# Performance work log

Measured on AMD Instinct MI355X. Metric: run time of the kernel, lower is better.

Reference implementation:

```python
import jax, jax.numpy as jnp
import numpy as np

N_SENT, B, S, D = 256, 512, 128, 1024
L, LATENT = 10331, 101  # int(sqrt(10331)) == 101


def setup_inputs() -> dict:
    key = jax.random.key(0)
    ks = jax.random.split(key, 16)
    inv = 1.0 / np.sqrt(D)
    return {
        'elmo_outputs': jax.random.normal(ks[0], (N_SENT, S, D), jnp.float32),
        'men_mask': jax.random.randint(ks[1], (B, S), 0, 2).astype(jnp.float32),
        'ctx_mask': jax.random.randint(ks[2], (B, S), 0, 2).astype(jnp.float32),
        'dist': jax.random.uniform(ks[3], (B, S), jnp.float32),
        'gathers': jax.random.randint(ks[4], (B,), 0, N_SENT),
        # nn.Linear weights, stored [out, in] as in torch
        'W_men_m': jax.random.normal(ks[5], (D, D), jnp.float32) * inv,
        'W_men_o': jax.random.normal(ks[6], (1, D), jnp.float32) * inv,
        'W_ctx_c': jax.random.normal(ks[7], (D, D), jnp.float32) * inv,
        'W_ctx_m': jax.random.normal(ks[8], (D, D), jnp.float32) * inv,
        'w_ctx_d': jax.random.normal(ks[9], (D,), jnp.float32),  # Linear(1, D) weight [D,1] squeezed
        'W_ctx_o': jax.random.normal(ks[10], (1, D), jnp.float32) * inv,
        'W_out': jax.random.normal(ks[11], (L, 2 * D), jnp.float32) * (1.0 / np.sqrt(2 * D)),
        'W_f2l': jax.random.normal(ks[12], (LATENT, 2 * D), jnp.float32) * (1.0 / np.sqrt(2 * D)),
        'W_l2l': jax.random.normal(ks[13], (L, LATENT), jnp.float32) * (1.0 / np.sqrt(LATENT)),
        'latent_scalar': jnp.array(0.1, jnp.float32),
    }


def reference(elmo_outputs, men_mask, ctx_mask, dist, gathers,
              W_men_m, W_men_o, W_ctx_c, W_ctx_m, w_ctx_d, W_ctx_o,
              W_out, W_f2l, W_l2l, latent_scalar):
    NEG = -10000.0
    # gather: sentence reps -> mention rows, [B, S, D]
    x = elmo_outputs[gathers]
    # mention additive attention
    men_h = jnp.tanh(jnp.einsum('bsd,ed->bse', x, W_men_m))
    men_score = jnp.einsum('bse,oe->bso', men_h, W_men_o)  # [B,S,1]
    men_score = men_score + (1.0 - men_mask[:, :, None]) * NEG
    men_attn = jax.nn.softmax(men_score, axis=1)
    men_repr = jnp.sum(x * men_attn, axis=1)  # [B, D]
    # context additive attention (dropout layers are identity in eval)
    ctx_h = jnp.tanh(
        jnp.einsum('bsd,ed->bse', x, W_ctx_c)
        + jnp.einsum('bd,ed->be', men_repr, W_ctx_m)[:, None, :]
        + dist[:, :, None] * w_ctx_d
    )
    ctx_score = jnp.einsum('bse,oe->bso', ctx_h, W_ctx_o)
    ctx_score = ctx_score + (1.0 - ctx_mask[:, :, None]) * NEG
    ctx_attn = jax.nn.softmax(ctx_score, axis=1)
    ctx_repr = jnp.sum(x * ctx_attn, axis=1)  # [B, D]
    final_repr = jnp.concatenate([men_repr, ctx_repr], axis=1)  # [B, 2D]
    outputs = final_repr @ W_out.T  # [B, L]
    latent_label = final_repr @ W_f2l.T  # [B, latent]
    outputs_latent = latent_label @ W_l2l.T  # [B, L]
    outputs = outputs + latent_scalar * outputs_latent
    return outputs, outputs_latent
```

## Files before the change

kernel.cpp:

```cpp
#include <hip/hip_runtime.h>
#include <hip/hip_bf16.h>

typedef __bf16 bf16x8 __attribute__((ext_vector_type(8)));
typedef float f32x4 __attribute__((ext_vector_type(4)));
typedef unsigned short u16x8 __attribute__((ext_vector_type(8)));

#define DEV __device__ __forceinline__

static constexpr int N_SENTC = 256, BB = 512, SS = 128, DD = 1024;
static constexpr int LL = 10331, LATENT = 101;
static constexpr int LPAD = 10368;
static constexpr int LATPAD = 128;

DEV float bf2f(unsigned short u) {
  unsigned v = (unsigned)u << 16;
  return __builtin_bit_cast(float, v);
}
DEV unsigned short f2bf(float f) {
  unsigned u = __builtin_bit_cast(unsigned, f);
  unsigned lsb = (u >> 16) & 1u;
  u += 0x7fffu + lsb;
  return (unsigned short)(u >> 16);
}

DEV void stage8(unsigned short* dst, const float* src) {
  float4 a = *(const float4*)src;
  float4 b = *(const float4*)(src + 4);
  unsigned short t[8];
  t[0] = f2bf(a.x); t[1] = f2bf(a.y); t[2] = f2bf(a.z); t[3] = f2bf(a.w);
  t[4] = f2bf(b.x); t[5] = f2bf(b.y); t[6] = f2bf(b.z); t[7] = f2bf(b.w);
  *(uint4*)dst = *(uint4*)t;
}

DEV void gl_lds16(const unsigned short* g, unsigned short* l) {
  __builtin_amdgcn_global_load_lds(
      (const __attribute__((address_space(1))) unsigned int*)g,
      (__attribute__((address_space(3))) unsigned int*)l, 16, 0, 0);
}

__global__ __launch_bounds__(256) void k_cvt(
    const float* __restrict__ src, unsigned short* __restrict__ dst, int n4) {
  for (int i = blockIdx.x * 256 + threadIdx.x; i < n4; i += gridDim.x * 256) {
    float4 v = ((const float4*)src)[i];
    unsigned short t[4] = {f2bf(v.x), f2bf(v.y), f2bf(v.z), f2bf(v.w)};
    ((uint2*)dst)[i] = *(const uint2*)t;
  }
}

__global__ __launch_bounds__(256) void k_cvt_pad(
    const float* __restrict__ src, unsigned short* __restrict__ dst,
    int srcR, int srcC, int dstC, int total) {
  for (int i = blockIdx.x * 256 + threadIdx.x; i < total; i += gridDim.x * 256) {
    int r = i / dstC, c = i - r * dstC;
    dst[i] = (r < srcR && c < srcC) ? f2bf(src[(size_t)r * srcC + c]) : (unsigned short)0;
  }
}

__global__ __launch_bounds__(512) void k_mc_gemm8(
    const unsigned short* __restrict__ Xb, const unsigned short* __restrict__ Wmb,
    const unsigned short* __restrict__ Wcb, const float* __restrict__ wo,
    float* __restrict__ score, unsigned short* __restrict__ Hc) {
  __shared__ __align__(16) unsigned short lds[2][2][2][8192];
  const int bid = blockIdx.x;
  const int lbid = (bid & 7) * 128 + (bid >> 3);
  const int colTile = lbid & 7, rowTile = lbid >> 3;
  const int rowBase = rowTile * 256;
  const bool isMen = colTile < 4;
  const unsigned short* __restrict__ Bsrc = isMen ? Wmb : Wcb;
  const int bcolBase = (colTile & 3) * 256;
  const int tid = threadIdx.x, w = tid >> 6, lane = tid & 63;
  const int lm = lane & 15, lq = lane >> 4;
  const int wr = w >> 2, wc = w & 3;
  const int stRow = w * 16 + (lane >> 2);
  const int stCol = ((lane & 3) * 8) ^ ((lane >> 5) << 4);
  const unsigned short* aSrc = Xb + (size_t)(rowBase + stRow) * 1024 + stCol;
  const unsigned short* bSrc = Bsrc + (size_t)(bcolBase + stRow) * 1024 + stCol;
  const int rdCol = (lq * 16) ^ ((lane & 8) ? 32 : 0);
  const int aoff = (wr * 16 + lm) * 64 + rdCol;
  const int boff = (wc * 16 + lm) * 64 + rdCol;
  f32x4 acc[8][4] = {};

  auto ST = [&](int op, int h, int kt, int buf) {
    const unsigned short* s = (op ? bSrc : aSrc) + (size_t)h * 131072 + kt * 64;
    unsigned short* d = &lds[buf][op][h][w * 512];
    gl_lds16(s, d);
    gl_lds16(s + 32, d + 4096);
  };

  ST(0, 0, 0, 0); ST(1, 0, 0, 0); ST(0, 1, 0, 0); ST(1, 1, 0, 0);
  ST(0, 0, 1, 1); ST(1, 0, 1, 1); ST(0, 1, 1, 1);
  asm volatile("s_waitcnt vmcnt(6)" ::: "memory");
  __builtin_amdgcn_s_barrier();

  bf16x8 af[4][2], bfr[4][2];
  for (int kt = 0; kt < 16; ++kt) {
    const int buf = kt & 1;
    const char* A0 = (const char*)&lds[buf][0][0][0];
    const char* A1 = (const char*)&lds[buf][0][1][0];
    const char* B0 = (const char*)&lds[buf][1][0][0];
    const char* B1 = (const char*)&lds[buf][1][1][0];
#pragma unroll
    for (int m = 0; m < 4; ++m)
#pragma unroll
      for (int ks = 0; ks < 2; ++ks)
        af[m][ks] = *(const bf16x8*)(A0 + aoff + m * 2048 + ks * 8192);
#pragma unroll
    for (int n = 0; n < 2; ++n)
#pragma unroll
      for (int ks = 0; ks < 2; ++ks)
        bfr[n][ks] = *(const bf16x8*)(B0 + boff + n * 4096 + ks * 8192);
    if (kt + 1 < 16) ST(1, 1, kt + 1, buf ^ 1);
    __builtin_amdgcn_s_barrier();
    __builtin_amdgcn_s_setprio(1);
#pragma unroll
    for (int m = 0; m < 4; ++m)
#pragma unroll
      for (int n = 0; n < 2; ++n)
#pragma unroll
        for (int ks = 0; ks < 2; ++ks)
          acc[m][n] = __builtin_amdgcn_mfma_f32_16x16x32_bf16(af[m][ks], bfr[n][ks], acc[m][n], 0, 0, 0);
    __builtin_amdgcn_s_setprio(0);
    __builtin_amdgcn_s_barrier();
#pragma unroll
    for (int n = 0; n < 2; ++n)
#pragma unroll
      for (int ks = 0; ks < 2; ++ks)
        bfr[2 + n][ks] = *(const bf16x8*)(B1 + boff + n * 4096 + ks * 8192);
    if (kt + 2 < 16) ST(0, 0, kt + 2, buf);
    __builtin_amdgcn_s_barrier();
    __builtin_amdgcn_s_setprio(1);
#pragma unroll
    for (int m = 0; m < 4; ++m)
#pragma unroll
      for (int n = 0; n < 2; ++n)
#pragma unroll
        for (int ks = 0; ks < 2; ++ks)
          acc[m][2 + n] = __builtin_amdgcn_mfma_f32_16x16x32_bf16(af[m][ks], bfr[2 + n][ks], acc[m][2 + n], 0, 0, 0);
    __builtin_amdgcn_s_setprio(0);
    __builtin_amdgcn_s_barrier();
#pragma unroll
    for (int m = 0; m < 4; ++m)
#pragma unroll
      for (int ks = 0; ks < 2; ++ks)
        af[m][ks] = *(const bf16x8*)(A1 + aoff + m * 2048 + ks * 8192);
    if (kt + 2 < 16) ST(1, 0, kt + 2, buf);
    __builtin_amdgcn_s_barrier();
    __builtin_amdgcn_s_setprio(1);
#pragma unroll
    for (int m = 0; m < 4; ++m)
#pragma unroll
      for (int n = 0; n < 2; ++n)
#pragma unroll
        for (int ks = 0; ks < 2; ++ks)
          acc[4 + m][n] = __builtin_amdgcn_mfma_f32_16x16x32_bf16(af[m][ks], bfr[n][ks], acc[4 + m][n], 0, 0, 0);
    __builtin_amdgcn_s_setprio(0);
    __builtin_amdgcn_s_barrier();
    if (kt + 2 < 16) ST(0, 1, kt + 2, buf);
    __builtin_amdgcn_s_barrier();
    __builtin_amdgcn_s_setprio(1);
#pragma unroll
    for (int m = 0; m < 4; ++m)
#pragma unroll
      for (int n = 0; n < 2; ++n)
#pragma unroll
        for (int ks = 0; ks < 2; ++ks)
          acc[4 + m][2 + n] = __builtin_amdgcn_mfma_f32_16x16x32_bf16(af[m][ks], bfr[2 + n][ks], acc[4 + m][2 + n], 0, 0, 0);
    __builtin_amdgcn_s_setprio(0);
    if (kt < 14) {
      asm volatile("s_waitcnt vmcnt(6)" ::: "memory");
    } else {
      asm volatile("s_waitcnt vmcnt(0)" ::: "memory");
    }
    __builtin_amdgcn_s_barrier();
  }

  if (isMen) {
    float wov[4];
#pragma unroll
    for (int n = 0; n < 4; ++n) wov[n] = wo[bcolBase + n * 64 + wc * 16 + lm];
    float rsum[8][4];
#pragma unroll
    for (int m = 0; m < 8; ++m)
#pragma unroll
      for (int r = 0; r < 4; ++r) {
        float s = 0.f;
#pragma unroll
        for (int n = 0; n < 4; ++n) s += tanhf(acc[m][n][r]) * wov[n];
        rsum[m][r] = s;
      }
#pragma unroll
    for (int msk = 1; msk <= 8; msk <<= 1)
#pragma unroll
      for (int m = 0; m < 8; ++m)
#pragma unroll
        for (int r = 0; r < 4; ++r) rsum[m][r] += __shfl_xor(rsum[m][r], msk, 64);
    if (lm == 0) {
#pragma unroll
      for (int m = 0; m < 8; ++m)
#pragma unroll
        for (int r = 0; r < 4; ++r)
          atomicAdd(&score[rowBase + m * 32 + wr * 16 + lq * 4 + r], rsum[m][r]);
    }
  } else {
    const int cb0 = (colTile - 4) * 256 + wc * 16 + lm;
#pragma unroll
    for (int m = 0; m < 8; ++m) {
      const int row = rowBase + m * 32 + wr * 16 + lq * 4;
#pragma unroll
      for (int n = 0; n < 4; ++n) {
        const int col = cb0 + n * 64;
#pragma unroll
        for (int r = 0; r < 4; ++r)
          Hc[(size_t)(row + r) * 1024 + col] = f2bf(acc[m][n][r]);
      }
    }
  }
}

__global__ __launch_bounds__(256) void k_ctx_score(
    const unsigned short* __restrict__ Hc, const int* __restrict__ gathers,
    const float* __restrict__ cb, const float* __restrict__ wd,
    const float* __restrict__ wo, const float* __restrict__ dist,
    float* __restrict__ score) {
  const int b = blockIdx.x, tid = threadIdx.x, wave = tid >> 6, lane = tid & 63;
  const int n = gathers[b];
  __shared__ float cbl[1024], wdl[1024], wol[1024];
  for (int i = tid; i < 1024; i += 256) {
    cbl[i] = cb[b * 1024 + i];
    wdl[i] = wd[i];
    wol[i] = wo[i];
  }
  __syncthreads();
  for (int s = wave; s < 128; s += 4) {
    float d = dist[b * 128 + s];
    const unsigned short* hrow = &Hc[(size_t)(n * 128 + s) * 1024 + lane * 16];
    unsigned short hs[16];
    *(uint4*)hs = *(const uint4*)hrow;
    *(uint4*)(hs + 8) = *(const uint4*)(hrow + 8);
    float p = 0.f;
#pragma unroll
    for (int j = 0; j < 16; ++j) {
      int e = lane * 16 + j;
      p += tanhf(bf2f(hs[j]) + cbl[e] + d * wdl[e]) * wol[e];
    }
#pragma unroll
    for (int msk = 1; msk <= 32; msk <<= 1) p += __shfl_xor(p, msk, 64);
    if (lane == 0) score[b * 128 + s] = p;
  }
}

__global__ __launch_bounds__(256) void k_softb(
    const float* __restrict__ score_src, const float* __restrict__ mask,
    const unsigned short* __restrict__ Xb, const int* __restrict__ gathers,
    unsigned short* __restrict__ finalrb, int isCtx) {
  const int b = blockIdx.x, tid = threadIdx.x;
  const int n = gathers[b];
  __shared__ float attn[128];
  __shared__ float red[128 * 8];
  __shared__ float smax, ssum;
  if (tid < 128) {
    int srow = isCtx ? b : n;
    attn[tid] = score_src[srow * 128 + tid] + (1.0f - mask[b * 128 + tid]) * (-10000.0f);
  }
  __syncthreads();
  if (tid == 0) {
    float m = attn[0];
    for (int i = 1; i < 128; ++i) m = fmaxf(m, attn[i]);
    smax = m;
  }
  __syncthreads();
  if (tid < 128) attn[tid] = expf(attn[tid] - smax);
  __syncthreads();
  if (tid == 0) {
    float s = 0.f;
    for (int i = 0; i < 128; ++i) s += attn[i];
    ssum = 1.0f / s;
  }
  __syncthreads();
  if (tid < 128) attn[tid] *= ssum;
  __syncthreads();
  const unsigned short* xb = Xb + (size_t)n * 128 * 1024;
  const int c = tid & 127, h = tid >> 7;
  float acc[8] = {};
  for (int s = h; s < 128; s += 2) {
    float w = attn[s];
    u16x8 v = *(const u16x8*)&xb[(size_t)s * 1024 + c * 8];
#pragma unroll
    for (int j = 0; j < 8; ++j) acc[j] += w * bf2f(v[j]);
  }
  if (h == 1) {
#pragma unroll
    for (int j = 0; j < 8; ++j) red[c * 8 + j] = acc[j];
  }
  __syncthreads();
  if (h == 0) {
    unsigned short o[8];
#pragma unroll
    for (int j = 0; j < 8; ++j) o[j] = f2bf(acc[j] + red[c * 8 + j]);
    *(uint4*)&finalrb[(size_t)b * 2048 + (isCtx ? 1024 : 0) + c * 8] = *(uint4*)o;
  }
}

__global__ __launch_bounds__(256) void k_cb_gemm_b(
    const unsigned short* __restrict__ finalrb, const unsigned short* __restrict__ Wcmb,
    float* __restrict__ cb) {
  __shared__ __align__(16) unsigned short As[64 * 32];
  __shared__ __align__(16) unsigned short Bs[64 * 32];
  const int bid = blockIdx.x;
  const int rowBase = (bid >> 4) * 64, colBase = (bid & 15) * 64;
  const int tid = threadIdx.x, wave = tid >> 6, lane = tid & 63;
  const int lm = lane & 15, lq = lane >> 4;
  const int sr = tid >> 2, sc = (tid & 3) * 8;
  f32x4 acc[4] = {};
  for (int k0 = 0; k0 < 1024; k0 += 32) {
    __syncthreads();
    *(uint4*)&As[sr * 32 + sc] = *(const uint4*)&finalrb[(size_t)(rowBase + sr) * 2048 + k0 + sc];
    *(uint4*)&Bs[sr * 32 + sc] = *(const uint4*)&Wcmb[(size_t)(colBase + sr) * 1024 + k0 + sc];
    __syncthreads();
    bf16x8 af = *(const bf16x8*)&As[(wave * 16 + lm) * 32 + lq * 8];
#pragma unroll
    for (int j = 0; j < 4; ++j) {
      bf16x8 bfr = *(const bf16x8*)&Bs[(j * 16 + lm) * 32 + lq * 8];
      acc[j] = __builtin_amdgcn_mfma_f32_16x16x32_bf16(af, bfr, acc[j], 0, 0, 0);
    }
  }
#pragma unroll
  for (int j = 0; j < 4; ++j) {
    int col = colBase + j * 16 + lm;
#pragma unroll
    for (int r = 0; r < 4; ++r) {
      int row = rowBase + wave * 16 + lq * 4 + r;
      cb[row * 1024 + col] = acc[j][r];
    }
  }
}

__global__ __launch_bounds__(256) void k_lat_gemm_b(
    const unsigned short* __restrict__ finalrb, const unsigned short* __restrict__ Wf2lb,
    unsigned short* __restrict__ latb) {
  __shared__ __align__(16) unsigned short As[64 * 32];
  __shared__ __align__(16) unsigned short Bs[64 * 32];
  const int rowBase = blockIdx.y * 64, colBase = blockIdx.x * 64;
  const int tid = threadIdx.x, wave = tid >> 6, lane = tid & 63;
  const int lm = lane & 15, lq = lane >> 4;
  const int sr = tid >> 2, sc = (tid & 3) * 8;
  f32x4 acc[4] = {};
  for (int k0 = 0; k0 < 2048; k0 += 32) {
    __syncthreads();
    *(uint4*)&As[sr * 32 + sc] = *(const uint4*)&finalrb[(size_t)(rowBase + sr) * 2048 + k0 + sc];
    *(uint4*)&Bs[sr * 32 + sc] = *(const uint4*)&Wf2lb[(size_t)(colBase + sr) * 2048 + k0 + sc];
    __syncthreads();
    bf16x8 af = *(const bf16x8*)&As[(wave * 16 + lm) * 32 + lq * 8];
#pragma unroll
    for (int j = 0; j < 4; ++j) {
      bf16x8 bfr = *(const bf16x8*)&Bs[(j * 16 + lm) * 32 + lq * 8];
      acc[j] = __builtin_amdgcn_mfma_f32_16x16x32_bf16(af, bfr, acc[j], 0, 0, 0);
    }
  }
#pragma unroll
  for (int j = 0; j < 4; ++j) {
    int col = colBase + j * 16 + lm;
#pragma unroll
    for (int r = 0; r < 4; ++r) {
      int row = rowBase + wave * 16 + lq * 4 + r;
      latb[row * LATPAD + col] = f2bf(acc[j][r]);
    }
  }
}

__global__ __launch_bounds__(256) void k_out_gemm_b(
    const unsigned short* __restrict__ finalrb, const unsigned short* __restrict__ Woutb,
    const unsigned short* __restrict__ latb, const unsigned short* __restrict__ Wl2lb,
    const float* __restrict__ lscale, float* __restrict__ out,
    float* __restrict__ outLat) {
  __shared__ __align__(16) unsigned short As[2 * 128 * 32];
  __shared__ __align__(16) unsigned short Bs[2 * 128 * 32];
  const int colBase = blockIdx.x * 128;
  const int rowBase = blockIdx.y * 128;
  const int tid = threadIdx.x, wave = tid >> 6, lane = tid & 63;
  const int lm = lane & 15, lq = lane >> 4;
  const int wr = (wave & 1) * 64, wc = (wave >> 1) * 64;
  const int srow = wave * 32 + (lane >> 2);
  const int scol = (lane & 3) * 8;
  const float scal = lscale[0];
  const unsigned short* aPtr = finalrb + (size_t)(rowBase + srow) * 2048 + scol;
  const unsigned short* bPtr = Woutb + (size_t)(colBase + srow) * 2048 + scol;
  f32x4 acc[4][4] = {};
  for (int k0 = 0; k0 < 2048; k0 += 64) {
    __syncthreads();
#pragma unroll
    for (int h = 0; h < 2; ++h) {
      gl_lds16(aPtr + k0 + h * 32, As + h * 4096 + wave * 1024);
      gl_lds16(aPtr + k0 + h * 32 + 16 * 2048, As + h * 4096 + wave * 1024 + 512);
      gl_lds16(bPtr + k0 + h * 32, Bs + h * 4096 + wave * 1024);
      gl_lds16(bPtr + k0 + h * 32 + 16 * 2048, Bs + h * 4096 + wave * 1024 + 512);
    }
    __syncthreads();
#pragma unroll
    for (int h = 0; h < 2; ++h) {
      bf16x8 af[4], bfr[4];
#pragma unroll
      for (int m = 0; m < 4; ++m)
        af[m] = *(const bf16x8*)&As[h * 4096 + (wr + m * 16 + lm) * 32 + lq * 8];
#pragma unroll
      for (int n = 0; n < 4; ++n)
        bfr[n] = *(const bf16x8*)&Bs[h * 4096 + (wc + n * 16 + lm) * 32 + lq * 8];
#pragma unroll
      for (int m = 0; m < 4; ++m)
#pragma unroll
        for (int n = 0; n < 4; ++n)
          acc[m][n] = __builtin_amdgcn_mfma_f32_16x16x32_bf16(af[m], bfr[n], acc[m][n], 0, 0, 0);
    }
  }
  const unsigned short* aPtr2 = latb + (size_t)(rowBase + srow) * LATPAD + scol;
  const unsigned short* bPtr2 = Wl2lb + (size_t)(colBase + srow) * LATPAD + scol;
  f32x4 acc2[4][4] = {};
  for (int k0 = 0; k0 < 128; k0 += 64) {
    __syncthreads();
#pragma unroll
    for (int h = 0; h < 2; ++h) {
      gl_lds16(aPtr2 + k0 + h * 32, As + h * 4096 + wave * 1024);
      gl_lds16(aPtr2 + k0 + h * 32 + 16 * LATPAD, As + h * 4096 + wave * 1024 + 512);
      gl_lds16(bPtr2 + k0 + h * 32, Bs + h * 4096 + wave * 1024);
      gl_lds16(bPtr2 + k0 + h * 32 + 16 * LATPAD, Bs + h * 4096 + wave * 1024 + 512);
    }
    __syncthreads();
#pragma unroll
    for (int h = 0; h < 2; ++h) {
      bf16x8 af[4], bfr[4];
#pragma unroll
      for (int m = 0; m < 4; ++m)
        af[m] = *(const bf16x8*)&As[h * 4096 + (wr + m * 16 + lm) * 32 + lq * 8];
#pragma unroll
      for (int n = 0; n < 4; ++n)
        bfr[n] = *(const bf16x8*)&Bs[h * 4096 + (wc + n * 16 + lm) * 32 + lq * 8];
#pragma unroll
      for (int m = 0; m < 4; ++m)
#pragma unroll
        for (int n = 0; n < 4; ++n)
          acc2[m][n] = __builtin_amdgcn_mfma_f32_16x16x32_bf16(af[m], bfr[n], acc2[m][n], 0, 0, 0);
    }
  }
#pragma unroll
  for (int m = 0; m < 4; ++m)
#pragma unroll
    for (int n = 0; n < 4; ++n) {
      int col = colBase + wc + n * 16 + lm;
      if (col < LL) {
#pragma unroll
        for (int r = 0; r < 4; ++r) {
          int row = rowBase + wr + m * 16 + lq * 4 + r;
          float lv = acc2[m][n][r];
          out[(size_t)row * LL + col] = acc[m][n][r] + scal * lv;
          outLat[(size_t)row * LL + col] = lv;
        }
      }
    }
}

__global__ __launch_bounds__(256) void k_men_gemm(
    const float* __restrict__ X, const float* __restrict__ Wm,
    const float* __restrict__ wo, float* __restrict__ score) {
  __shared__ __align__(16) unsigned short As[64 * 32];
  __shared__ __align__(16) unsigned short Bs[64 * 32];
  const int bid = blockIdx.x;
  const int rowBase = (bid >> 4) * 64, colBase = (bid & 15) * 64;
  const int tid = threadIdx.x, wave = tid >> 6, lane = tid & 63;
  const int lm = lane & 15, lq = lane >> 4;
  const int sr = tid >> 2, sc = (tid & 3) * 8;
  f32x4 acc[4] = {};
  for (int k0 = 0; k0 < 1024; k0 += 32) {
    __syncthreads();
    stage8(&As[sr * 32 + sc], &X[(size_t)(rowBase + sr) * 1024 + k0 + sc]);
    stage8(&Bs[sr * 32 + sc], &Wm[(size_t)(colBase + sr) * 1024 + k0 + sc]);
    __syncthreads();
    bf16x8 af = *(const bf16x8*)&As[(wave * 16 + lm) * 32 + lq * 8];
#pragma unroll
    for (int j = 0; j < 4; ++j) {
      bf16x8 bfr = *(const bf16x8*)&Bs[(j * 16 + lm) * 32 + lq * 8];
      acc[j] = __builtin_amdgcn_mfma_f32_16x16x32_bf16(af, bfr, acc[j], 0, 0, 0);
    }
  }
  float rsum[4] = {0.f, 0.f, 0.f, 0.f};
#pragma unroll
  for (int j = 0; j < 4; ++j) {
    float w = wo[colBase + j * 16 + lm];
#pragma unroll
    for (int r = 0; r < 4; ++r) rsum[r] += tanhf(acc[j][r]) * w;
  }
#pragma unroll
  for (int m = 1; m <= 8; m <<= 1)
#pragma unroll
    for (int r = 0; r < 4; ++r) rsum[r] += __shfl_xor(rsum[r], m, 64);
  if (lm == 0) {
    int row0 = rowBase + wave * 16 + lq * 4;
#pragma unroll
    for (int r = 0; r < 4; ++r) atomicAdd(&score[row0 + r], rsum[r]);
  }
}

__global__ __launch_bounds__(256) void k_ctx_gemm(
    const float* __restrict__ X, const int* __restrict__ gathers,
    const float* __restrict__ Wc, const float* __restrict__ wd,
    const float* __restrict__ wo, const float* __restrict__ dist,
    const float* __restrict__ cb, float* __restrict__ score) {
  __shared__ __align__(16) unsigned short As[64 * 32];
  __shared__ __align__(16) unsigned short Bs[64 * 32];
  const int bid = blockIdx.x;
  const int rowBase = (bid >> 4) * 64, colBase = (bid & 15) * 64;
  const int tid = threadIdx.x, wave = tid >> 6, lane = tid & 63;
  const int lm = lane & 15, lq = lane >> 4;
  const int sr = tid >> 2, sc = (tid & 3) * 8;
  const int row_g = rowBase + sr;
  const int srcRow = (gathers[row_g >> 7] << 7) + (row_g & 127);
  f32x4 acc[4] = {};
  for (int k0 = 0; k0 < 1024; k0 += 32) {
    __syncthreads();
    stage8(&As[sr * 32 + sc], &X[(size_t)srcRow * 1024 + k0 + sc]);
    stage8(&Bs[sr * 32 + sc], &Wc[(size_t)(colBase + sr) * 1024 + k0 + sc]);
    __syncthreads();
    bf16x8 af = *(const bf16x8*)&As[(wave * 16 + lm) * 32 + lq * 8];
#pragma unroll
    for (int j = 0; j < 4; ++j) {
      bf16x8 bfr = *(const bf16x8*)&Bs[(j * 16 + lm) * 32 + lq * 8];
      acc[j] = __builtin_amdgcn_mfma_f32_16x16x32_bf16(af, bfr, acc[j], 0, 0, 0);
    }
  }
  float rsum[4] = {0.f, 0.f, 0.f, 0.f};
#pragma unroll
  for (int j = 0; j < 4; ++j) {
    int col = colBase + j * 16 + lm;
    float w = wo[col];
    float wdv = wd[col];
#pragma unroll
    for (int r = 0; r < 4; ++r) {
      int rg = rowBase + wave * 16 + lq * 4 + r;
      int b = rg >> 7, s = rg & 127;
      float v = acc[j][r] + cb[b * 1024 + col] + dist[b * 128 + s] * wdv;
      rsum[r] += tanhf(v) * w;
    }
  }
#pragma unroll
  for (int m = 1; m <= 8; m <<= 1)
#pragma unroll
    for (int r = 0; r < 4; ++r) rsum[r] += __shfl_xor(rsum[r], m, 64);
  if (lm == 0) {
    int row0 = rowBase + wave * 16 + lq * 4;
#pragma unroll
    for (int r = 0; r < 4; ++r) atomicAdd(&score[row0 + r], rsum[r]);
  }
}

__global__ __launch_bounds__(256) void k_soft(
    const float* __restrict__ score_src, const float* __restrict__ mask,
    const float* __restrict__ X, const int* __restrict__ gathers,
    float* __restrict__ finalr, int isCtx) {
  const int b = blockIdx.x, tid = threadIdx.x;
  const int n = gathers[b];
  __shared__ float attn[128];
  __shared__ float smax, ssum;
  if (tid < 128) {
    int srow = isCtx ? b : n;
    attn[tid] = score_src[srow * 128 + tid] + (1.0f - mask[b * 128 + tid]) * (-10000.0f);
  }
  __syncthreads();
  if (tid == 0) {
    float m = attn[0];
    for (int i = 1; i < 128; ++i) m = fmaxf(m, attn[i]);
    smax = m;
  }
  __syncthreads();
  if (tid < 128) attn[tid] = expf(attn[tid] - smax);
  __syncthreads();
  if (tid == 0) {
    float s = 0.f;
    for (int i = 0; i < 128; ++i) s += attn[i];
    ssum = 1.0f / s;
  }
  __syncthreads();
  if (tid < 128) attn[tid] *= ssum;
  __syncthreads();
  const float* xb = &X[(size_t)(n << 7) * 1024];
  const int off = isCtx ? 1024 : 0;
  for (int d = tid; d < 1024; d += 256) {
    float a = 0.f;
#pragma unroll 8
    for (int s = 0; s < 128; ++s) a += attn[s] * xb[s * 1024 + d];
    finalr[b * 2048 + off + d] = a;
  }
}

__global__ __launch_bounds__(256) void k_cb_gemm(
    const float* __restrict__ finalr, const float* __restrict__ Wcm,
    float* __restrict__ cb) {
  __shared__ __align__(16) unsigned short As[64 * 32];
  __shared__ __align__(16) unsigned short Bs[64 * 32];
  const int bid = blockIdx.x;
  const int rowBase = (bid >> 4) * 64, colBase = (bid & 15) * 64;
  const int tid = threadIdx.x, wave = tid >> 6, lane = tid & 63;
  const int lm = lane & 15, lq = lane >> 4;
  const int sr = tid >> 2, sc = (tid & 3) * 8;
  f32x4 acc[4] = {};
  for (int k0 = 0; k0 < 1024; k0 += 32) {
    __syncthreads();
    stage8(&As[sr * 32 + sc], &finalr[(size_t)(rowBase + sr) * 2048 + k0 + sc]);
    stage8(&Bs[sr * 32 + sc], &Wcm[(size_t)(colBase + sr) * 1024 + k0 + sc]);
    __syncthreads();
    bf16x8 af = *(const bf16x8*)&As[(wave * 16 + lm) * 32 + lq * 8];
#pragma unroll
    for (int j = 0; j < 4; ++j) {
      bf16x8 bfr = *(const bf16x8*)&Bs[(j * 16 + lm) * 32 + lq * 8];
      acc[j] = __builtin_amdgcn_mfma_f32_16x16x32_bf16(af, bfr, acc[j], 0, 0, 0);
    }
  }
#pragma unroll
  for (int j = 0; j < 4; ++j) {
    int col = colBase + j * 16 + lm;
#pragma unroll
    for (int r = 0; r < 4; ++r) {
      int row = rowBase + wave * 16 + lq * 4 + r;
      cb[row * 1024 + col] = acc[j][r];
    }
  }
}

__global__ __launch_bounds__(256) void k_lat_gemm(
    const float* __restrict__ finalr, const float* __restrict__ Wf2l,
    float* __restrict__ lat) {
  __shared__ __align__(16) unsigned short As[64 * 32];
  __shared__ __align__(16) unsigned short Bs[64 * 32];
  const int rowBase = blockIdx.y * 64, colBase = blockIdx.x * 64;
  const int tid = threadIdx.x, wave = tid >> 6, lane = tid & 63;
  const int lm = lane & 15, lq = lane >> 4;
  const int sr = tid >> 2, sc = (tid & 3) * 8;
  f32x4 acc[4] = {};
  for (int k0 = 0; k0 < 2048; k0 += 32) {
    __syncthreads();
    stage8(&As[sr * 32 + sc], &finalr[(size_t)(rowBase + sr) * 2048 + k0 + sc]);
    int l = colBase + sr;
    if (l < LATENT) {
      stage8(&Bs[sr * 32 + sc], &Wf2l[(size_t)l * 2048 + k0 + sc]);
    } else {
      uint4 z = {0, 0, 0, 0};
      *(uint4*)&Bs[sr * 32 + sc] = z;
    }
    __syncthreads();
    bf16x8 af = *(const bf16x8*)&As[(wave * 16 + lm) * 32 + lq * 8];
#pragma unroll
    for (int j = 0; j < 4; ++j) {
      bf16x8 bfr = *(const bf16x8*)&Bs[(j * 16 + lm) * 32 + lq * 8];
      acc[j] = __builtin_amdgcn_mfma_f32_16x16x32_bf16(af, bfr, acc[j], 0, 0, 0);
    }
  }
#pragma unroll
  for (int j = 0; j < 4; ++j) {
    int col = colBase + j * 16 + lm;
    if (col < LATENT) {
#pragma unroll
      for (int r = 0; r < 4; ++r) {
        int row = rowBase + wave * 16 + lq * 4 + r;
        lat[row * LATENT + col] = acc[j][r];
      }
    }
  }
}

__global__ __launch_bounds__(256) void k_out_gemm(
    const float* __restrict__ finalr, const float* __restrict__ Wout,
    const float* __restrict__ lat, const float* __restrict__ Wl2l,
    const float* __restrict__ lscale, float* __restrict__ out,
    float* __restrict__ outLat) {
  __shared__ __align__(16) unsigned short As[64 * 32];
  __shared__ __align__(16) unsigned short Bs[64 * 32];
  const int rowBase = blockIdx.y * 64, colBase = blockIdx.x * 64;
  const int tid = threadIdx.x, wave = tid >> 6, lane = tid & 63;
  const int lm = lane & 15, lq = lane >> 4;
  const int sr = tid >> 2, sc = (tid & 3) * 8;
  const float scal = lscale[0];
  const int lrow = colBase + sr;
  const bool lvalid = (lrow < LL);
  f32x4 acc[4] = {};
  for (int k0 = 0; k0 < 2048; k0 += 32) {
    __syncthreads();
    stage8(&As[sr * 32 + sc], &finalr[(size_t)(rowBase + sr) * 2048 + k0 + sc]);
    if (lvalid) {
      stage8(&Bs[sr * 32 + sc], &Wout[(size_t)lrow * 2048 + k0 + sc]);
    } else {
      uint4 z = {0, 0, 0, 0};
      *(uint4*)&Bs[sr * 32 + sc] = z;
    }
    __syncthreads();
    bf16x8 af = *(const bf16x8*)&As[(wave * 16 + lm) * 32 + lq * 8];
#pragma unroll
    for (int j = 0; j < 4; ++j) {
      bf16x8 bfr = *(const bf16x8*)&Bs[(j * 16 + lm) * 32 + lq * 8];
      acc[j] = __builtin_amdgcn_mfma_f32_16x16x32_bf16(af, bfr, acc[j], 0, 0, 0);
    }
  }
  f32x4 acc2[4] = {};
  for (int k2 = 0; k2 < 128; k2 += 32) {
    __syncthreads();
    const int brow = rowBase + sr;
#pragma unroll
    for (int jj = 0; jj < 8; ++jj) {
      int idx = k2 + sc + jj;
      As[sr * 32 + sc + jj] = (idx < LATENT) ? f2bf(lat[brow * LATENT + idx]) : (unsigned short)0;
      Bs[sr * 32 + sc + jj] = (lvalid && idx < LATENT) ? f2bf(Wl2l[lrow * LATENT + idx]) : (unsigned short)0;
    }
    __syncthreads();
    bf16x8 af = *(const bf16x8*)&As[(wave * 16 + lm) * 32 + lq * 8];
#pragma unroll
    for (int j = 0; j < 4; ++j) {
      bf16x8 bfr = *(const bf16x8*)&Bs[(j * 16 + lm) * 32 + lq * 8];
      acc2[j] = __builtin_amdgcn_mfma_f32_16x16x32_bf16(af, bfr, acc2[j], 0, 0, 0);
    }
  }
#pragma unroll
  for (int j = 0; j < 4; ++j) {
    int col = colBase + j * 16 + lm;
    if (col < LL) {
#pragma unroll
      for (int r = 0; r < 4; ++r) {
        int row = rowBase + wave * 16 + lq * 4 + r;
        float lv = acc2[j][r];
        out[(size_t)row * LL + col] = acc[j][r] + scal * lv;
        outLat[(size_t)row * LL + col] = lv;
      }
    }
  }
}

extern "C" void kernel_launch(void* const* d_in, const int* in_sizes, int n_in,
                              void* d_out, int out_size, void* d_ws, size_t ws_size,
                              hipStream_t stream) {
  const float* X = (const float*)d_in[0];
  const float* men_mask = (const float*)d_in[1];
  const float* ctx_mask = (const float*)d_in[2];
  const float* dist = (const float*)d_in[3];
  const int* gathers = (const int*)d_in[4];
  const float* W_men_m = (const float*)d_in[5];
  const float* W_men_o = (const float*)d_in[6];
  const float* W_ctx_c = (const float*)d_in[7];
  const float* W_ctx_m = (const float*)d_in[8];
  const float* w_ctx_d = (const float*)d_in[9];
  const float* W_ctx_o = (const float*)d_in[10];
  const float* W_out = (const float*)d_in[11];
  const float* W_f2l = (const float*)d_in[12];
  const float* W_l2l = (const float*)d_in[13];
  const float* lscale = (const float*)d_in[14];
  float* out = (float*)d_out;
  float* outLat = out + (size_t)BB * LL;

  size_t off = 0;
  auto carve = [&](size_t bytes) {
    void* p = (char*)d_ws + off;
    off = (off + bytes + 255) & ~(size_t)255;
    return p;
  };
  float* sent_score = (float*)carve(32768 * 4);
  float* ctx_score = (float*)carve(65536 * 4);
  float* finalr = (float*)carve((size_t)512 * 2048 * 4);
  float* cb = (float*)carve((size_t)512 * 1024 * 4);
  float* lat = (float*)carve((size_t)512 * LATENT * 4);
  unsigned short* Xb = (unsigned short*)carve((size_t)32768 * 1024 * 2);
  unsigned short* Wmb = (unsigned short*)carve((size_t)1024 * 1024 * 2);
  unsigned short* Wcb = (unsigned short*)carve((size_t)1024 * 1024 * 2);
  unsigned short* Wcmb = (unsigned short*)carve((size_t)1024 * 1024 * 2);
  unsigned short* Hc = (unsigned short*)carve((size_t)32768 * 1024 * 2);
  unsigned short* Wf2lb = (unsigned short*)carve((size_t)LATPAD * 2048 * 2);
  unsigned short* Wl2lb = (unsigned short*)carve((size_t)LPAD * LATPAD * 2);
  unsigned short* finalrb = (unsigned short*)carve((size_t)512 * 2048 * 2);
  unsigned short* latb = (unsigned short*)carve((size_t)512 * LATPAD * 2);
  const bool fits = off <= ws_size;
  unsigned short* Woutb = Xb;

  if (fits) {
    hipMemsetAsync(sent_score, 0, 32768 * sizeof(float), stream);
    k_cvt<<<8192, 256, 0, stream>>>(X, Xb, 32768 * 1024 / 4);
    k_cvt<<<1024, 256, 0, stream>>>(W_men_m, Wmb, 1024 * 1024 / 4);
    k_cvt<<<1024, 256, 0, stream>>>(W_ctx_c, Wcb, 1024 * 1024 / 4);
    k_cvt<<<1024, 256, 0, stream>>>(W_ctx_m, Wcmb, 1024 * 1024 / 4);
    k_cvt_pad<<<512, 256, 0, stream>>>(W_f2l, Wf2lb, LATENT, 2048, 2048, LATPAD * 2048);
    k_cvt_pad<<<1024, 256, 0, stream>>>(W_l2l, Wl2lb, LL, LATENT, LATPAD, LPAD * LATPAD);
    k_mc_gemm8<<<1024, 512, 0, stream>>>(Xb, Wmb, Wcb, W_men_o, sent_score, Hc);
    k_softb<<<512, 256, 0, stream>>>(sent_score, men_mask, Xb, gathers, finalrb, 0);
    k_cb_gemm_b<<<128, 256, 0, stream>>>(finalrb, Wcmb, cb);
    k_ctx_score<<<512, 256, 0, stream>>>(Hc, gathers, cb, w_ctx_d, W_ctx_o, dist, ctx_score);
    k_softb<<<512, 256, 0, stream>>>(ctx_score, ctx_mask, Xb, gathers, finalrb, 1);
    k_lat_gemm_b<<<dim3(2, 8), 256, 0, stream>>>(finalrb, Wf2lb, latb);
    k_cvt_pad<<<8192, 256, 0, stream>>>(W_out, Woutb, LL, 2048, 2048, LPAD * 2048);
    k_out_gemm_b<<<dim3(81, 4), 256, 0, stream>>>(finalrb, Woutb, latb, Wl2lb,
                                                  lscale, out, outLat);
  } else {
    hipMemsetAsync(d_ws, 0, (32768 + 65536) * sizeof(float), stream);
    k_men_gemm<<<8192, 256, 0, stream>>>(X, W_men_m, W_men_o, sent_score);
    k_soft<<<512, 256, 0, stream>>>(sent_score, men_mask, X, gathers, finalr, 0);
    k_cb_gemm<<<128, 256, 0, stream>>>(finalr, W_ctx_m, cb);
    k_ctx_gemm<<<16384, 256, 0, stream>>>(X, gathers, W_ctx_c, w_ctx_d, W_ctx_o, dist, cb, ctx_score);
    k_soft<<<512, 256, 0, stream>>>(ctx_score, ctx_mask, X, gathers, finalr, 1);
    k_lat_gemm<<<dim3(2, 8), 256, 0, stream>>>(finalr, W_f2l, lat);
    k_out_gemm<<<dim3(162, 8), 256, 0, stream>>>(finalr, W_out, lat, W_l2l, lscale, out, outLat);
  }
}
```

Baseline: 708.9 us.

## Make mention/context GEMM persistent over four tiles and use fast tanh

```diff
diff --git a/kernel.cpp b/kernel.cpp
--- a/kernel.cpp
+++ b/kernel.cpp
@@ -21,6 +21,11 @@
   unsigned lsb = (u >> 16) & 1u;
   u += 0x7fffu + lsb;
   return (unsigned short)(u >> 16);
+}
+
+DEV float fast_tanh(float x) {
+  float e = __expf(2.0f * x);
+  return 1.0f - 2.0f / (e + 1.0f);
 }
 
 DEV void stage8(unsigned short* dst, const float* src) {
@@ -61,24 +66,30 @@
     const unsigned short* __restrict__ Wcb, const float* __restrict__ wo,
     float* __restrict__ score, unsigned short* __restrict__ Hc) {
   __shared__ __align__(16) unsigned short lds[2][2][2][8192];
-  const int bid = blockIdx.x;
-  const int lbid = (bid & 7) * 128 + (bid >> 3);
-  const int colTile = lbid & 7, rowTile = lbid >> 3;
-  const int rowBase = rowTile * 256;
-  const bool isMen = colTile < 4;
-  const unsigned short* __restrict__ Bsrc = isMen ? Wmb : Wcb;
-  const int bcolBase = (colTile & 3) * 256;
+  const int p = blockIdx.x;
   const int tid = threadIdx.x, w = tid >> 6, lane = tid & 63;
   const int lm = lane & 15, lq = lane >> 4;
   const int wr = w >> 2, wc = w & 3;
   const int stRow = w * 16 + (lane >> 2);
   const int stCol = ((lane & 3) * 8) ^ ((lane >> 5) << 4);
-  const unsigned short* aSrc = Xb + (size_t)(rowBase + stRow) * 1024 + stCol;
-  const unsigned short* bSrc = Bsrc + (size_t)(bcolBase + stRow) * 1024 + stCol;
   const int rdCol = (lq * 16) ^ ((lane & 8) ? 32 : 0);
   const int aoff = (wr * 16 + lm) * 64 + rdCol;
   const int boff = (wc * 16 + lm) * 64 + rdCol;
-  f32x4 acc[8][4] = {};
+
+  const unsigned short* aSrc;
+  const unsigned short* bSrc;
+  int rowBase, bcolBase;
+  bool isMen;
+  auto setTile = [&](int t) {
+    const int vbid = p + 256 * t;
+    const int lbid = (vbid & 7) * 128 + (vbid >> 3);
+    const int colTile = lbid & 7, rowTile = lbid >> 3;
+    rowBase = rowTile * 256;
+    isMen = colTile < 4;
+    bcolBase = (colTile & 3) * 256;
+    aSrc = Xb + (size_t)(rowBase + stRow) * 1024 + stCol;
+    bSrc = (isMen ? Wmb : Wcb) + (size_t)(bcolBase + stRow) * 1024 + stCol;
+  };
 
   auto ST = [&](int op, int h, int kt, int buf) {
     const unsigned short* s = (op ? bSrc : aSrc) + (size_t)h * 131072 + kt * 64;
@@ -86,133 +97,145 @@
     gl_lds16(s, d);
     gl_lds16(s + 32, d + 4096);
   };
-
-  ST(0, 0, 0, 0); ST(1, 0, 0, 0); ST(0, 1, 0, 0); ST(1, 1, 0, 0);
-  ST(0, 0, 1, 1); ST(1, 0, 1, 1); ST(0, 1, 1, 1);
-  asm volatile("s_waitcnt vmcnt(6)" ::: "memory");
-  __builtin_amdgcn_s_barrier();
-
-  bf16x8 af[4][2], bfr[4][2];
-  for (int kt = 0; kt < 16; ++kt) {
-    const int buf = kt & 1;
-    const char* A0 = (const char*)&lds[buf][0][0][0];
-    const char* A1 = (const char*)&lds[buf][0][1][0];
-    const char* B0 = (const char*)&lds[buf][1][0][0];
-    const char* B1 = (const char*)&lds[buf][1][1][0];
-#pragma unroll
-    for (int m = 0; m < 4; ++m)
-#pragma unroll
-      for (int ks = 0; ks < 2; ++ks)
-        af[m][ks] = *(const bf16x8*)(A0 + aoff + m * 2048 + ks * 8192);
-#pragma unroll
-    for (int n = 0; n < 2; ++n)
-#pragma unroll
-      for (int ks = 0; ks < 2; ++ks)
-        bfr[n][ks] = *(const bf16x8*)(B0 + boff + n * 4096 + ks * 8192);
-    if (kt + 1 < 16) ST(1, 1, kt + 1, buf ^ 1);
+  auto PRO = [&]() {
+    ST(0, 0, 0, 0); ST(1, 0, 0, 0); ST(0, 1, 0, 0); ST(1, 1, 0, 0);
+    ST(0, 0, 1, 1); ST(1, 0, 1, 1); ST(0, 1, 1, 1);
+  };
+
+  setTile(0);
+  PRO();
+
+  for (int t = 0; t < 4; ++t) {
+    asm volatile("s_waitcnt vmcnt(6)" ::: "memory");
     __builtin_amdgcn_s_barrier();
-    __builtin_amdgcn_s_setprio(1);
-#pragma unroll
-    for (int m = 0; m < 4; ++m)
+
+    f32x4 acc[8][4] = {};
+    bf16x8 af0[4][2], af1[4][2], bfr[4][2];
+    for (int kt = 0; kt < 16; ++kt) {
+      const int buf = kt & 1;
+      const char* A0 = (const char*)&lds[buf][0][0][0];
+      const char* A1 = (const char*)&lds[buf][0][1][0];
+      const char* B0 = (const char*)&lds[buf][1][0][0];
+      const char* B1 = (const char*)&lds[buf][1][1][0];
+#pragma unroll
+      for (int m = 0; m < 4; ++m)
+#pragma unroll
+        for (int ks = 0; ks < 2; ++ks)
+          af0[m][ks] = *(const bf16x8*)(A0 + aoff + m * 2048 + ks * 8192);
 #pragma unroll
       for (int n = 0; n < 2; ++n)
 #pragma unroll
         for (int ks = 0; ks < 2; ++ks)
-          acc[m][n] = __builtin_amdgcn_mfma_f32_16x16x32_bf16(af[m][ks], bfr[n][ks], acc[m][n], 0, 0, 0);
-    __builtin_amdgcn_s_setprio(0);
-    __builtin_amdgcn_s_barrier();
-#pragma unroll
-    for (int n = 0; n < 2; ++n)
-#pragma unroll
-      for (int ks = 0; ks < 2; ++ks)
-        bfr[2 + n][ks] = *(const bf16x8*)(B1 + boff + n * 4096 + ks * 8192);
-    if (kt + 2 < 16) ST(0, 0, kt + 2, buf);
-    __builtin_amdgcn_s_barrier();
-    __builtin_amdgcn_s_setprio(1);
-#pragma unroll
-    for (int m = 0; m < 4; ++m)
+          bfr[n][ks] = *(const bf16x8*)(B0 + boff + n * 4096 + ks * 8192);
+      if (kt + 1 < 16) ST(1, 1, kt + 1, buf ^ 1);
+      __builtin_amdgcn_s_barrier();
+      __builtin_amdgcn_s_setprio(1);
+#pragma unroll
+      for (int m = 0; m < 4; ++m)
+#pragma unroll
+        for (int n = 0; n < 2; ++n)
+#pragma unroll
+          for (int ks = 0; ks < 2; ++ks)
+            acc[m][n] = __builtin_amdgcn_mfma_f32_16x16x32_bf16(af0[m][ks], bfr[n][ks], acc[m][n], 0, 0, 0);
+      __builtin_amdgcn_s_setprio(0);
+      __builtin_amdgcn_s_barrier();
 #pragma unroll
       for (int n = 0; n < 2; ++n)
 #pragma unroll
         for (int ks = 0; ks < 2; ++ks)
-          acc[m][2 + n] = __builtin_amdgcn_mfma_f32_16x16x32_bf16(af[m][ks], bfr[2 + n][ks], acc[m][2 + n], 0, 0, 0);
-    __builtin_amdgcn_s_setprio(0);
-    __builtin_amdgcn_s_barrier();
-#pragma unroll
-    for (int m = 0; m < 4; ++m)
-#pragma unroll
-      for (int ks = 0; ks < 2; ++ks)
-        af[m][ks] = *(const bf16x8*)(A1 + aoff + m * 2048 + ks * 8192);
-    if (kt + 2 < 16) ST(1, 0, kt + 2, buf);
-    __builtin_amdgcn_s_barrier();
-    __builtin_amdgcn_s_setprio(1);
-#pragma unroll
-    for (int m = 0; m < 4; ++m)
-#pragma unroll
-      for (int n = 0; n < 2; ++n)
+          bfr[2 + n][ks] = *(const bf16x8*)(B1 + boff + n * 4096 + ks * 8192);
+      if (kt + 2 < 16) ST(0, 0, kt + 2, buf);
+      __builtin_amdgcn_s_barrier();
+      __builtin_amdgcn_s_setprio(1);
+#pragma unroll
+      for (int m = 0; m < 4; ++m)
+#pragma unroll
+        for (int n = 0; n < 2; ++n)
+#pragma unroll
+          for (int ks = 0; ks < 2; ++ks)
+            acc[m][2 + n] = __builtin_amdgcn_mfma_f32_16x16x32_bf16(af0[m][ks], bfr[2 + n][ks], acc[m][2 + n], 0, 0, 0);
+      __builtin_amdgcn_s_setprio(0);
+      __builtin_amdgcn_s_barrier();
+#pragma unroll
+      for (int m = 0; m < 4; ++m)
 #pragma unroll
         for (int ks = 0; ks < 2; ++ks)
-          acc[4 + m][n] = __builtin_amdgcn_mfma_f32_16x16x32_bf16(af[m][ks], bfr[n][ks], acc[4 + m][n], 0, 0, 0);
-    __builtin_amdgcn_s_setprio(0);
-    __builtin_amdgcn_s_barrier();
-    if (kt + 2 < 16) ST(0, 1, kt + 2, buf);
-    __builtin_amdgcn_s_barrier();
-    __builtin_amdgcn_s_setprio(1);
-#pragma unroll
-    for (int m = 0; m < 4; ++m)
-#pragma unroll
-      for (int n = 0; n < 2; ++n)
-#pragma unroll
-        for (int ks = 0; ks < 2; ++ks)
-          acc[4 + m][2 + n] = __builtin_amdgcn_mfma_f32_16x16x32_bf16(af[m][ks], bfr[2 + n][ks], acc[4 + m][2 + n], 0, 0, 0);
-    __builtin_amdgcn_s_setprio(0);
-    if (kt < 14) {
-      asm volatile("s_waitcnt vmcnt(6)" ::: "memory");
+          af1[m][ks] = *(const bf16x8*)(A1 + aoff + m * 2048 + ks * 8192);
+      if (kt + 2 < 16) ST(1, 0, kt + 2, buf);
+      __builtin_amdgcn_s_barrier();
+      __builtin_amdgcn_s_setprio(1);
+#pragma unroll
+      for (int m = 0; m < 4; ++m)
+#pragma unroll
+        for (int n = 0; n < 2; ++n)
+#pragma unroll
+          for (int ks = 0; ks < 2; ++ks)
+            acc[4 + m][n] = __builtin_amdgcn_mfma_f32_16x16x32_bf16(af1[m][ks], bfr[n][ks], acc[4 + m][n], 0, 0, 0);
+      __builtin_amdgcn_s_setprio(0);
+      __builtin_amdgcn_s_barrier();
+      if (kt + 2 < 16) ST(0, 1, kt + 2, buf);
+      __builtin_amdgcn_s_barrier();
+      __builtin_amdgcn_s_setprio(1);
+#pragma unroll
+      for (int m = 0; m < 4; ++m)
+#pragma unroll
+        for (int n = 0; n < 2; ++n)
+#pragma unroll
+          for (int ks = 0; ks < 2; ++ks)
+            acc[4 + m][2 + n] = __builtin_amdgcn_mfma_f32_16x16x32_bf16(af1[m][ks], bfr[2 + n][ks], acc[4 + m][2 + n], 0, 0, 0);
+      __builtin_amdgcn_s_setprio(0);
+      if (kt < 14) {
+        asm volatile("s_waitcnt vmcnt(6)" ::: "memory");
+      } else {
+        asm volatile("s_waitcnt vmcnt(0)" ::: "memory");
+      }
+      __builtin_amdgcn_s_barrier();
+    }
+
+    if (isMen) {
+      float wov[4];
+#pragma unroll
+      for (int n = 0; n < 4; ++n) wov[n] = wo[bcolBase + n * 64 + wc * 16 + lm];
+      float rsum[8][4];
+#pragma unroll
+      for (int m = 0; m < 8; ++m)
+#pragma unroll
+        for (int r = 0; r < 4; ++r) {
+          float s = 0.f;
+#pragma unroll
+          for (int n = 0; n < 4; ++n) s += fast_tanh(acc[m][n][r]) * wov[n];
+          rsum[m][r] = s;
+        }
+#pragma unroll
+      for (int msk = 1; msk <= 8; msk <<= 1)
+#pragma unroll
+        for (int m = 0; m < 8; ++m)
+#pragma unroll
+          for (int r = 0; r < 4; ++r) rsum[m][r] += __shfl_xor(rsum[m][r], msk, 64);
+      if (lm == 0) {
+#pragma unroll
+        for (int m = 0; m < 8; ++m)
+#pragma unroll
+          for (int r = 0; r < 4; ++r)
+            atomicAdd(&score[rowBase + m * 32 + wr * 16 + lq * 4 + r], rsum[m][r]);
+      }
     } else {
-      asm volatile("s_waitcnt vmcnt(0)" ::: "memory");
-    }
-    __builtin_amdgcn_s_barrier();
-  }
-
-  if (isMen) {
-    float wov[4];
-#pragma unroll
-    for (int n = 0; n < 4; ++n) wov[n] = wo[bcolBase + n * 64 + wc * 16 + lm];
-    float rsum[8][4];
-#pragma unroll
-    for (int m = 0; m < 8; ++m)
-#pragma unroll
-      for (int r = 0; r < 4; ++r) {
-        float s = 0.f;
-#pragma unroll
-        for (int n = 0; n < 4; ++n) s += tanhf(acc[m][n][r]) * wov[n];
-        rsum[m][r] = s;
+      const int cb0 = bcolBase + wc * 16 + lm;
+#pragma unroll
+      for (int m = 0; m < 8; ++m) {
+        const int row = rowBase + m * 32 + wr * 16 + lq * 4;
+#pragma unroll
+        for (int n = 0; n < 4; ++n) {
+          const int col = cb0 + n * 64;
+#pragma unroll
+          for (int r = 0; r < 4; ++r)
+            Hc[(size_t)(row + r) * 1024 + col] = f2bf(acc[m][n][r]);
+        }
       }
-#pragma unroll
-    for (int msk = 1; msk <= 8; msk <<= 1)
-#pragma unroll
-      for (int m = 0; m < 8; ++m)
-#pragma unroll
-        for (int r = 0; r < 4; ++r) rsum[m][r] += __shfl_xor(rsum[m][r], msk, 64);
-    if (lm == 0) {
-#pragma unroll
-      for (int m = 0; m < 8; ++m)
-#pragma unroll
-        for (int r = 0; r < 4; ++r)
-          atomicAdd(&score[rowBase + m * 32 + wr * 16 + lq * 4 + r], rsum[m][r]);
-    }
-  } else {
-    const int cb0 = (colTile - 4) * 256 + wc * 16 + lm;
-#pragma unroll
-    for (int m = 0; m < 8; ++m) {
-      const int row = rowBase + m * 32 + wr * 16 + lq * 4;
-#pragma unroll
-      for (int n = 0; n < 4; ++n) {
-        const int col = cb0 + n * 64;
-#pragma unroll
-        for (int r = 0; r < 4; ++r)
-          Hc[(size_t)(row + r) * 1024 + col] = f2bf(acc[m][n][r]);
-      }
+    }
+    if (t < 3) {
+      setTile(t + 1);
+      PRO();
     }
   }
 }
@@ -241,7 +264,7 @@
 #pragma unroll
     for (int j = 0; j < 16; ++j) {
       int e = lane * 16 + j;
-      p += tanhf(bf2f(hs[j]) + cbl[e] + d * wdl[e]) * wol[e];
+      p += fast_tanh(bf2f(hs[j]) + cbl[e] + d * wdl[e]) * wol[e];
     }
 #pragma unroll
     for (int msk = 1; msk <= 32; msk <<= 1) p += __shfl_xor(p, msk, 64);
@@ -782,7 +805,7 @@
     k_cvt<<<1024, 256, 0, stream>>>(W_ctx_m, Wcmb, 1024 * 1024 / 4);
     k_cvt_pad<<<512, 256, 0, stream>>>(W_f2l, Wf2lb, LATENT, 2048, 2048, LATPAD * 2048);
     k_cvt_pad<<<1024, 256, 0, stream>>>(W_l2l, Wl2lb, LL, LATENT, LATPAD, LPAD * LATPAD);
-    k_mc_gemm8<<<1024, 512, 0, stream>>>(Xb, Wmb, Wcb, W_men_o, sent_score, Hc);
+    k_mc_gemm8<<<256, 512, 0, stream>>>(Xb, Wmb, Wcb, W_men_o, sent_score, Hc);
     k_softb<<<512, 256, 0, stream>>>(sent_score, men_mask, Xb, gathers, finalrb, 0);
     k_cb_gemm_b<<<128, 256, 0, stream>>>(finalrb, Wcmb, cb);
     k_ctx_score<<<512, 256, 0, stream>>>(Hc, gathers, cb, w_ctx_d, W_ctx_o, dist, ctx_score);
```

Result: faster. 662.6 us (-6.5%).
